# Kernel optimization log

Hardware: AMD Instinct MI355X
Metric: run time of the kernel (lower is better)

The kernel has to match this reference:

```python
import jax, jax.numpy as jnp
import numpy as np

NEG_SLOPE = 0.1
BN_EPS = 1e-5
STD_EPS = 1e-5


def leaky_relu(x):
    return jnp.where(x >= 0, x, NEG_SLOPE * x)


def conv_bn_act(x, w, gamma, beta):
    # Conv1d(kernel_size=1, bias=False) + BatchNorm1d (train-mode batch stats) + LeakyReLU(0.1)
    y = jnp.einsum('bcn,oc->bon', x, w)
    m = y.mean(axis=(0, 2), keepdims=True)
    v = y.var(axis=(0, 2), keepdims=True)  # biased, as torch BN
    y = (y - m) / jnp.sqrt(v + BN_EPS) * gamma[None, :, None] + beta[None, :, None]
    return leaky_relu(y)


def knn_idx(x, k):
    # x: [B, C, N]; faithful to torch knn(): topk(k+1) of negative squared distance, then keep first k (includes self)
    xx = jnp.sum(x * x, axis=1, keepdims=True)            # [B, 1, N]
    inner = -2.0 * jnp.einsum('bcn,bcm->bnm', x, x)       # [B, N, N]
    pd = -xx - inner - jnp.swapaxes(xx, 1, 2)             # [B, N, N]
    _, idx = jax.lax.top_k(pd, k + 1)
    return idx[:, :, :k]


def setup_inputs() -> dict:
    key = jax.random.key(0)
    ks = jax.random.split(key, 4)
    B, C, N, O = 8, 3, 4096, 32
    return {
        'xyz': jax.random.normal(ks[0], (B, C, N), dtype=jnp.float32),
        'w_nn': jax.random.normal(ks[1], (O, C), dtype=jnp.float32) * 0.1,
        'alpha': jnp.ones((1, 1, 1, O), dtype=jnp.float32),
        'beta_a': jnp.zeros((1, 1, 1, O), dtype=jnp.float32),
        'w0': jax.random.normal(ks[2], (O, C), dtype=jnp.float32) * 0.1,
        'g0': jnp.ones((O,), dtype=jnp.float32),
        'b0': jnp.zeros((O,), dtype=jnp.float32),
        'w1': jax.random.normal(ks[3], (O, O), dtype=jnp.float32) * 0.1,
        'g1': jnp.ones((O,), dtype=jnp.float32),
        'b1': jnp.zeros((O,), dtype=jnp.float32),
        'k': 16,
    }


def reference(xyz, w_nn, alpha, beta_a, w0, g0, b0, w1, g1, b1, k):
    # MLP branch on raw channels
    x = conv_bn_act(xyz, w0, g0, b0)
    x = conv_bn_act(x, w1, g1, b1)          # [B, 32, N]

    # KNN + gather neighbors
    idx = knn_idx(xyz, k)                   # [B, N, k]
    pts = jnp.swapaxes(xyz, 1, 2)           # [B, N, C]
    grouped = jax.vmap(lambda p, i: p[i])(pts, idx)  # [B, N, k, C]

    # neighbor_normal: diff -> 1x1 conv -> global-std normalize -> affine
    res = grouped - pts[:, :, None, :]
    res = jnp.einsum('bnkc,oc->bnko', res, w_nn)      # [B, N, k, 32]
    B = res.shape[0]
    std = jnp.std(res.reshape(B, -1), axis=-1, ddof=1).reshape(B, 1, 1, 1)  # torch.std is unbiased
    gp = alpha * (res / (std + STD_EPS)) + beta_a

    # max over neighbors, to [B, 32, N]
    gp = jnp.swapaxes(gp.max(axis=2), 1, 2)

    point_feature = jnp.concatenate([x, gp], axis=1)  # [B, 64, N]
    return point_feature, idx
```

## Files before the change

kernel.cpp:

```cpp
#include <hip/hip_runtime.h>
#include <stdint.h>

#define B_  8
#define N_  4096
#define O_  32
#define K_  16
#define BN_ (B_ * N_)
#define PF_ (B_ * 64 * N_)
#define CB_ 256
#define RPB 4
#define CHUNK 1024

enum : int {
  WS_PARTA = 0,
  WS_XX    = 1024,
  WS_SC0   = WS_XX + BN_,
  WS_SH0   = WS_SC0 + 32,
  WS_PARTC = WS_SH0 + 32,
  WS_SC1   = WS_PARTC + 4096,
  WS_SH1   = WS_SC1 + 32,
  WS_MAXV  = WS_SH1 + 32,
  WS_MINV  = WS_MAXV + BN_ * 32,
  WS_ROWS  = WS_MINV + BN_ * 32,
  WS_DEN   = WS_ROWS + BN_ * 2,
  WS_TOTAL = WS_DEN + 8
};
#define WS_PARTC2 WS_MAXV

__global__ __launch_bounds__(256) void kA(const float* __restrict__ xyz,
                                          float* __restrict__ ws) {
  int tid = threadIdx.x;
  int gid = blockIdx.x * 256 + tid;
  float s0 = 0.f, s1 = 0.f, s2 = 0.f;
  float m00 = 0.f, m01 = 0.f, m02 = 0.f, m11 = 0.f, m12 = 0.f, m22 = 0.f;
  for (int i = gid; i < BN_; i += 64 * 256) {
    int b = i >> 12, n = i & (N_ - 1);
    const float* xb = xyz + b * 3 * N_;
    float x0 = xb[n], x1 = xb[N_ + n], x2 = xb[2 * N_ + n];
    float xx = __fadd_rn(__fadd_rn(__fmul_rn(x0, x0), __fmul_rn(x1, x1)),
                         __fmul_rn(x2, x2));
    ws[WS_XX + i] = xx;
    s0 += x0; s1 += x1; s2 += x2;
    m00 = fmaf(x0, x0, m00); m01 = fmaf(x0, x1, m01); m02 = fmaf(x0, x2, m02);
    m11 = fmaf(x1, x1, m11); m12 = fmaf(x1, x2, m12); m22 = fmaf(x2, x2, m22);
  }
  __shared__ float sd[256];
  float acc[9] = {s0, s1, s2, m00, m01, m02, m11, m12, m22};
#pragma unroll
  for (int q = 0; q < 9; ++q) {
    sd[tid] = acc[q];
    __syncthreads();
    for (int s = 128; s > 0; s >>= 1) {
      if (tid < s) sd[tid] += sd[tid + s];
      __syncthreads();
    }
    if (tid == 0) ws[WS_PARTA + blockIdx.x * 9 + q] = sd[0];
    __syncthreads();
  }
}

__global__ __launch_bounds__(64) void kB(const float* __restrict__ w0,
                                         const float* __restrict__ g0,
                                         const float* __restrict__ b0,
                                         float* __restrict__ ws) {
  __shared__ float S[9];
  int tid = threadIdx.x;
  if (tid < 9) {
    float s = 0.f;
    for (int blk = 0; blk < 64; ++blk) s += ws[WS_PARTA + blk * 9 + tid];
    S[tid] = s;
  }
  __syncthreads();
  if (tid < 32) {
    const float inv = 1.0f / 32768.0f;
    float mc0 = S[0] * inv, mc1 = S[1] * inv, mc2 = S[2] * inv;
    float M00 = S[3] * inv, M01 = S[4] * inv, M02 = S[5] * inv;
    float M11 = S[6] * inv, M12 = S[7] * inv, M22 = S[8] * inv;
    float w0c = w0[tid * 3], w1c = w0[tid * 3 + 1], w2c = w0[tid * 3 + 2];
    float m = w0c * mc0 + w1c * mc1 + w2c * mc2;
    float e2 = w0c * w0c * M00 + w1c * w1c * M11 + w2c * w2c * M22 +
               2.f * (w0c * w1c * M01 + w0c * w2c * M02 + w1c * w2c * M12);
    float v = fmaxf(e2 - m * m, 0.f);
    float sc = g0[tid] / sqrtf(v + 1e-5f);
    ws[WS_SC0 + tid] = sc;
    ws[WS_SH0 + tid] = b0[tid] - m * sc;
  }
}

__global__ __launch_bounds__(256) void kC(const float* __restrict__ xyz,
                                          const float* __restrict__ w0,
                                          const float* __restrict__ w1,
                                          float* __restrict__ ws) {
  __shared__ float w0s[96], sc0s[32], sh0s[32], w1s[32 * 33], xs[8][33], red[256];
  int tid = threadIdx.x;
  if (tid < 96) w0s[tid] = w0[tid];
  if (tid < 32) { sc0s[tid] = ws[WS_SC0 + tid]; sh0s[tid] = ws[WS_SH0 + tid]; }
  for (int i = tid; i < 1024; i += 256) w1s[(i >> 5) * 33 + (i & 31)] = w1[i];
  __syncthreads();
  int p = tid >> 5, o = tid & 31;
  float S = 0.f, S2 = 0.f;
  for (int it = 0; it < 16; ++it) {
    int i = blockIdx.x * 128 + it * 8 + p;
    int b = i >> 12, n = i & (N_ - 1);
    const float* xb = xyz + b * 3 * N_;
    float x0 = xb[n], x1 = xb[N_ + n], x2 = xb[2 * N_ + n];
    float y0 = x0 * w0s[o * 3] + x1 * w0s[o * 3 + 1] + x2 * w0s[o * 3 + 2];
    float a = y0 * sc0s[o] + sh0s[o];
    xs[p][o] = (a >= 0.f) ? a : 0.1f * a;
    __syncthreads();
    float y1 = 0.f;
#pragma unroll
    for (int c = 0; c < 32; ++c) y1 = fmaf(w1s[o * 33 + c], xs[p][c], y1);
    S += y1; S2 = fmaf(y1, y1, S2);
    __syncthreads();
  }
  red[tid] = S;
  __syncthreads();
  if (p == 0) {
    float t = 0.f;
    for (int pp = 0; pp < 8; ++pp) t += red[pp * 32 + o];
    ws[WS_PARTC2 + blockIdx.x * 64 + o] = t;
  }
  __syncthreads();
  red[tid] = S2;
  __syncthreads();
  if (p == 0) {
    float t = 0.f;
    for (int pp = 0; pp < 8; ++pp) t += red[pp * 32 + o];
    ws[WS_PARTC2 + blockIdx.x * 64 + 32 + o] = t;
  }
}

__global__ __launch_bounds__(64) void kD(const float* __restrict__ g1,
                                         const float* __restrict__ b1,
                                         float* __restrict__ ws) {
  int o = threadIdx.x;
  if (o >= 32) return;
  float S = 0.f, S2 = 0.f;
  for (int blk = 0; blk < CB_; ++blk) {
    S += ws[WS_PARTC2 + blk * 64 + o];
    S2 += ws[WS_PARTC2 + blk * 64 + 32 + o];
  }
  float m = S / 32768.f;
  float v = fmaxf(S2 / 32768.f - m * m, 0.f);
  float sc = g1[o] / sqrtf(v + 1e-5f);
  ws[WS_SC1 + o] = sc;
  ws[WS_SH1 + o] = b1[o] - m * sc;
}

__global__ __launch_bounds__(256) void kE(const float* __restrict__ xyz,
                                          const float* __restrict__ w0,
                                          const float* __restrict__ w1,
                                          const float* __restrict__ ws,
                                          float* __restrict__ out) {
  __shared__ float w0s[96], sc0s[32], sh0s[32], sc1s[32], sh1s[32], w1s[32 * 33],
      xs[8][33];
  int tid = threadIdx.x;
  if (tid < 96) w0s[tid] = w0[tid];
  if (tid < 32) {
    sc0s[tid] = ws[WS_SC0 + tid]; sh0s[tid] = ws[WS_SH0 + tid];
    sc1s[tid] = ws[WS_SC1 + tid]; sh1s[tid] = ws[WS_SH1 + tid];
  }
  for (int i = tid; i < 1024; i += 256) w1s[(i >> 5) * 33 + (i & 31)] = w1[i];
  __syncthreads();
  int p = tid >> 5, o = tid & 31;
  int o2 = tid >> 3, p2 = tid & 7;
  for (int it = 0; it < 16; ++it) {
    int i = blockIdx.x * 128 + it * 8 + p;
    int b = i >> 12, n = i & (N_ - 1);
    const float* xb = xyz + b * 3 * N_;
    float x0 = xb[n], x1 = xb[N_ + n], x2 = xb[2 * N_ + n];
    float y0 = x0 * w0s[o * 3] + x1 * w0s[o * 3 + 1] + x2 * w0s[o * 3 + 2];
    float a = y0 * sc0s[o] + sh0s[o];
    xs[p][o] = (a >= 0.f) ? a : 0.1f * a;
    __syncthreads();
    float y1 = 0.f;
#pragma unroll
    for (int c = 0; c < 32; ++c) y1 = fmaf(w1s[o * 33 + c], xs[p][c], y1);
    float z = y1 * sc1s[o] + sh1s[o];
    float x1v = (z >= 0.f) ? z : 0.1f * z;
    __syncthreads();
    xs[p][o] = x1v;
    __syncthreads();
    int i2 = blockIdx.x * 128 + it * 8 + p2;
    int b2 = i2 >> 12, n2 = i2 & (N_ - 1);
    out[b2 * 64 * N_ + o2 * N_ + n2] = xs[p2][o2];
    __syncthreads();
  }
}

__global__ __launch_bounds__(256) void kF(const float* __restrict__ xyz,
                                          const float* __restrict__ w_nn,
                                          float* __restrict__ out,
                                          float* __restrict__ ws) {
  int wave = threadIdx.x >> 6, lane = threadIdx.x & 63;
  int row = blockIdx.x * RPB + wave;
  int b = row >> 12, n = row & (N_ - 1);
  const float* xb = xyz + b * 3 * N_;
  const float* xxp = ws + WS_XX + b * N_;
  float qx = xb[n], qy = xb[N_ + n], qz = xb[2 * N_ + n];
  float xxn = xxp[n];

  __shared__ float sx[CHUNK], sy[CHUNK], sz[CHUNK], sxx[CHUNK];
  __shared__ unsigned long long list[RPB][64];
  __shared__ float rb[RPB][16][33];

  unsigned keys[64];
  unsigned umin = 0xFFFFFFFFu;
#pragma unroll
  for (int c = 0; c < N_ / CHUNK; ++c) {
    int cb = c * CHUNK;
    __syncthreads();
#pragma unroll
    for (int t = 0; t < CHUNK / (RPB * 64); ++t) {
      int i = t * (RPB * 64) + threadIdx.x;
      sx[i] = xb[cb + i];
      sy[i] = xb[N_ + cb + i];
      sz[i] = xb[2 * N_ + cb + i];
      sxx[i] = xxp[cb + i];
    }
    __syncthreads();
#pragma unroll
    for (int jj = 0; jj < CHUNK / 64; ++jj) {
      int ml = (jj << 6) | lane;
      float px = sx[ml], py = sy[ml], pz = sz[ml];
      float dot = __fmaf_rn(pz, qz, __fmaf_rn(py, qy, __fmul_rn(px, qx)));
      float inner = __fmul_rn(-2.0f, dot);
      float t = __fsub_rn(-sxx[ml], inner);
      float pn = __fsub_rn(xxn, t);
      unsigned u = __float_as_uint(pn);
      u ^= ((unsigned)((int)u >> 31)) | 0x80000000u;
      keys[c * (CHUNK / 64) + jj] = u;
      umin = (u < umin) ? u : umin;
    }
  }

  unsigned e = umin;
#pragma unroll
  for (int k = 2; k <= 64; k <<= 1) {
#pragma unroll
    for (int d = k >> 1; d >= 1; d >>= 1) {
      unsigned pe = __shfl_xor(e, d, 64);
      bool up = ((lane & k) == 0);
      bool lower = ((lane & d) == 0);
      unsigned lo = (e < pe) ? e : pe;
      unsigned hi = (e < pe) ? pe : e;
      e = (up == lower) ? lo : hi;
    }
  }
  unsigned T = __shfl(e, 15, 64);

  list[wave][lane] = ~0ull;
  __syncthreads();
  int base = 0;
#pragma unroll
  for (int j = 0; j < 64; ++j) {
    bool pred = (keys[j] <= T);
    unsigned long long mask = __ballot(pred);
    if (mask != 0ull) {
      if (pred) {
        int rank = __popcll(mask & ((1ull << lane) - 1ull));
        int slot = base + rank;
        if (slot < 64)
          list[wave][slot] = ((unsigned long long)keys[j] << 32) |
                             (unsigned)((j << 6) | lane);
      }
      base += __popcll(mask);
    }
  }
  __syncthreads();

  unsigned long long ev = list[wave][lane];
#pragma unroll
  for (int k = 2; k <= 64; k <<= 1) {
#pragma unroll
    for (int d = k >> 1; d >= 1; d >>= 1) {
      unsigned long long pe = __shfl_xor(ev, d, 64);
      bool up = ((lane & k) == 0);
      bool lower = ((lane & d) == 0);
      bool lt = (ev < pe);
      unsigned long long lo = lt ? ev : pe;
      unsigned long long hi = lt ? pe : ev;
      ev = (up == lower) ? lo : hi;
    }
  }
  int m = (int)(unsigned)(ev & 0xffffffffull);
  if (lane < 16) out[PF_ + row * 16 + lane] = (float)m;

  float s = 0.f, s2 = 0.f;
  if (lane < 16) {
    float dx = __fsub_rn(xb[m], qx);
    float dy = __fsub_rn(xb[N_ + m], qy);
    float dz = __fsub_rn(xb[2 * N_ + m], qz);
#pragma unroll
    for (int o = 0; o < 32; ++o) {
      float r = __fmaf_rn(dz, w_nn[o * 3 + 2],
                __fmaf_rn(dy, w_nn[o * 3 + 1], __fmul_rn(dx, w_nn[o * 3])));
      rb[wave][lane][o] = r;
      s += r;
      s2 = __fmaf_rn(r, r, s2);
    }
  }
  __syncthreads();
  if (lane < 32) {
    float mx = -__builtin_inff(), mn = __builtin_inff();
#pragma unroll
    for (int r = 0; r < 16; ++r) {
      float v = rb[wave][r][lane];
      mx = fmaxf(mx, v);
      mn = fminf(mn, v);
    }
    ws[WS_MAXV + row * 32 + lane] = mx;
    ws[WS_MINV + row * 32 + lane] = mn;
  }
#pragma unroll
  for (int off = 1; off < 64; off <<= 1) {
    s += __shfl_xor(s, off, 64);
    s2 += __shfl_xor(s2, off, 64);
  }
  if (lane == 0) {
    ws[WS_ROWS + row * 2] = s;
    ws[WS_ROWS + row * 2 + 1] = s2;
  }
}

__global__ __launch_bounds__(256) void kG(float* __restrict__ ws) {
  int b = blockIdx.x, tid = threadIdx.x;
  float s = 0.f, s2 = 0.f;
  for (int i = tid; i < N_; i += 256) {
    s += ws[WS_ROWS + (b * N_ + i) * 2];
    s2 += ws[WS_ROWS + (b * N_ + i) * 2 + 1];
  }
  __shared__ float sd[256], sd2[256];
  sd[tid] = s; sd2[tid] = s2;
  __syncthreads();
  for (int st = 128; st > 0; st >>= 1) {
    if (tid < st) { sd[tid] += sd[tid + st]; sd2[tid] += sd2[tid + st]; }
    __syncthreads();
  }
  if (tid == 0) {
    const float M = 2097152.0f;
    float var = fmaxf((sd2[0] - sd[0] * (sd[0] / M)) / (M - 1.0f), 0.f);
    ws[WS_DEN + b] = sqrtf(var) + 1e-5f;
  }
}

__global__ __launch_bounds__(256) void kH(const float* __restrict__ alpha,
                                          const float* __restrict__ beta,
                                          const float* __restrict__ ws,
                                          float* __restrict__ out) {
  int i = blockIdx.x * 256 + threadIdx.x;
  if (i >= B_ * 32 * N_) return;
  int n = i & (N_ - 1);
  int o = (i >> 12) & 31;
  int b = i >> 17;
  float denom = ws[WS_DEN + b];
  float al = alpha[o], be = beta[o];
  int base = (b * N_ + n) * 32 + o;
  float v = (al >= 0.f) ? ws[WS_MAXV + base] : ws[WS_MINV + base];
  out[b * 64 * N_ + (32 + o) * N_ + n] = __fadd_rn(__fmul_rn(al, v / denom), be);
}

extern "C" void kernel_launch(void* const* d_in, const int* in_sizes, int n_in,
                              void* d_out, int out_size, void* d_ws, size_t ws_size,
                              hipStream_t stream) {
  const float* xyz   = (const float*)d_in[0];
  const float* w_nn  = (const float*)d_in[1];
  const float* alpha = (const float*)d_in[2];
  const float* beta_a= (const float*)d_in[3];
  const float* w0    = (const float*)d_in[4];
  const float* g0    = (const float*)d_in[5];
  const float* b0    = (const float*)d_in[6];
  const float* w1    = (const float*)d_in[7];
  const float* g1    = (const float*)d_in[8];
  const float* b1    = (const float*)d_in[9];
  float* out = (float*)d_out;
  float* ws  = (float*)d_ws;

  kA<<<64, 256, 0, stream>>>(xyz, ws);
  kB<<<1, 64, 0, stream>>>(w0, g0, b0, ws);
  kC<<<CB_, 256, 0, stream>>>(xyz, w0, w1, ws);
  kD<<<1, 64, 0, stream>>>(g1, b1, ws);
  kE<<<CB_, 256, 0, stream>>>(xyz, w0, w1, ws, out);
  kF<<<BN_ / RPB, RPB * 64, 0, stream>>>(xyz, w_nn, out, ws);
  kG<<<B_, 256, 0, stream>>>(ws);
  kH<<<(B_ * 32 * N_ + 255) / 256, 256, 0, stream>>>(alpha, beta_a, ws, out);
}
```

Measured before the change: 170.4 us.

## Double-buffer KNN point chunks via register prefetch and keep float keys

```diff
diff --git a/kernel.cpp b/kernel.cpp
--- a/kernel.cpp
+++ b/kernel.cpp
@@ -9,7 +9,8 @@
 #define PF_ (B_ * 64 * N_)
 #define CB_ 256
 #define RPB 4
-#define CHUNK 1024
+#define CHK 512
+#define NCHK (N_ / CHK)
 
 enum : int {
   WS_PARTA = 0,
@@ -193,7 +194,8 @@
                                           const float* __restrict__ w_nn,
                                           float* __restrict__ out,
                                           float* __restrict__ ws) {
-  int wave = threadIdx.x >> 6, lane = threadIdx.x & 63;
+  int tid = threadIdx.x;
+  int wave = tid >> 6, lane = tid & 63;
   int row = blockIdx.x * RPB + wave;
   int b = row >> 12, n = row & (N_ - 1);
   const float* xb = xyz + b * 3 * N_;
@@ -201,41 +203,52 @@
   float qx = xb[n], qy = xb[N_ + n], qz = xb[2 * N_ + n];
   float xxn = xxp[n];
 
-  __shared__ float sx[CHUNK], sy[CHUNK], sz[CHUNK], sxx[CHUNK];
+  __shared__ float sx[2][CHK], sy[2][CHK], sz[2][CHK], sxx[2][CHK];
   __shared__ unsigned long long list[RPB][64];
   __shared__ float rb[RPB][16][33];
 
-  unsigned keys[64];
-  unsigned umin = 0xFFFFFFFFu;
-#pragma unroll
-  for (int c = 0; c < N_ / CHUNK; ++c) {
-    int cb = c * CHUNK;
-    __syncthreads();
-#pragma unroll
-    for (int t = 0; t < CHUNK / (RPB * 64); ++t) {
-      int i = t * (RPB * 64) + threadIdx.x;
-      sx[i] = xb[cb + i];
-      sy[i] = xb[N_ + cb + i];
-      sz[i] = xb[2 * N_ + cb + i];
-      sxx[i] = xxp[cb + i];
-    }
-    __syncthreads();
-#pragma unroll
-    for (int jj = 0; jj < CHUNK / 64; ++jj) {
+  float keys[64];
+  float mn = __builtin_inff();
+  float rx0, rx1, ry0, ry1, rz0, rz1, rw0, rw1;
+  rx0 = xb[tid];           rx1 = xb[tid + 256];
+  ry0 = xb[N_ + tid];      ry1 = xb[N_ + tid + 256];
+  rz0 = xb[2 * N_ + tid];  rz1 = xb[2 * N_ + tid + 256];
+  rw0 = xxp[tid];          rw1 = xxp[tid + 256];
+#pragma unroll
+  for (int c = 0; c < NCHK; ++c) {
+    int buf = c & 1;
+    sx[buf][tid] = rx0;  sx[buf][tid + 256] = rx1;
+    sy[buf][tid] = ry0;  sy[buf][tid + 256] = ry1;
+    sz[buf][tid] = rz0;  sz[buf][tid + 256] = rz1;
+    sxx[buf][tid] = rw0; sxx[buf][tid + 256] = rw1;
+    __syncthreads();
+    if (c + 1 < NCHK) {
+      int i0 = (c + 1) * CHK + tid;
+      rx0 = xb[i0];           rx1 = xb[i0 + 256];
+      ry0 = xb[N_ + i0];      ry1 = xb[N_ + i0 + 256];
+      rz0 = xb[2 * N_ + i0];  rz1 = xb[2 * N_ + i0 + 256];
+      rw0 = xxp[i0];          rw1 = xxp[i0 + 256];
+    }
+#pragma unroll
+    for (int jj = 0; jj < CHK / 64; ++jj) {
       int ml = (jj << 6) | lane;
-      float px = sx[ml], py = sy[ml], pz = sz[ml];
+      float px = sx[buf][ml], py = sy[buf][ml], pz = sz[buf][ml];
       float dot = __fmaf_rn(pz, qz, __fmaf_rn(py, qy, __fmul_rn(px, qx)));
       float inner = __fmul_rn(-2.0f, dot);
-      float t = __fsub_rn(-sxx[ml], inner);
+      float t = __fsub_rn(-sxx[buf][ml], inner);
       float pn = __fsub_rn(xxn, t);
-      unsigned u = __float_as_uint(pn);
-      u ^= ((unsigned)((int)u >> 31)) | 0x80000000u;
-      keys[c * (CHUNK / 64) + jj] = u;
-      umin = (u < umin) ? u : umin;
-    }
-  }
-
-  unsigned e = umin;
+      keys[c * (CHK / 64) + jj] = pn;
+      mn = fminf(mn, pn);
+    }
+    __syncthreads();
+  }
+
+  unsigned e;
+  {
+    unsigned u = __float_as_uint(mn);
+    u ^= ((unsigned)((int)u >> 31)) | 0x80000000u;
+    e = u;
+  }
 #pragma unroll
   for (int k = 2; k <= 64; k <<= 1) {
 #pragma unroll
@@ -248,7 +261,9 @@
       e = (up == lower) ? lo : hi;
     }
   }
-  unsigned T = __shfl(e, 15, 64);
+  unsigned tm = __shfl(e, 15, 64);
+  unsigned tfu = (tm & 0x80000000u) ? (tm ^ 0x80000000u) : ~tm;
+  float T = __uint_as_float(tfu);
 
   list[wave][lane] = ~0ull;
   __syncthreads();
@@ -259,10 +274,12 @@
     unsigned long long mask = __ballot(pred);
     if (mask != 0ull) {
       if (pred) {
+        unsigned uu = __float_as_uint(keys[j]);
+        uu ^= ((unsigned)((int)uu >> 31)) | 0x80000000u;
         int rank = __popcll(mask & ((1ull << lane) - 1ull));
         int slot = base + rank;
         if (slot < 64)
-          list[wave][slot] = ((unsigned long long)keys[j] << 32) |
+          list[wave][slot] = ((unsigned long long)uu << 32) |
                              (unsigned)((j << 6) | lane);
       }
       base += __popcll(mask);
@@ -303,15 +320,15 @@
   }
   __syncthreads();
   if (lane < 32) {
-    float mx = -__builtin_inff(), mn = __builtin_inff();
+    float mx = -__builtin_inff(), mnv = __builtin_inff();
 #pragma unroll
     for (int r = 0; r < 16; ++r) {
       float v = rb[wave][r][lane];
       mx = fmaxf(mx, v);
-      mn = fminf(mn, v);
+      mnv = fminf(mnv, v);
     }
     ws[WS_MAXV + row * 32 + lane] = mx;
-    ws[WS_MINV + row * 32 + lane] = mn;
+    ws[WS_MINV + row * 32 + lane] = mnv;
   }
 #pragma unroll
   for (int off = 1; off < 64; off <<= 1) {
```

After: 155.9 us. 1.09x faster.
